# Performance work log

Hardware: AMD Instinct MI355X
Metric: run time of the kernel (lower is better)

The kernel has to match this reference:

```python
import jax, jax.numpy as jnp
import numpy as np

GWIDTH2 = 0.3  # Gaussian bandwidth squared
PNORM = 2


def setup_inputs() -> dict:
    key = jax.random.key(0)
    k1, k2 = jax.random.split(key)
    b, c, h, w = 16, 3, 256, 256
    npro = 32
    x = jax.random.uniform(k1, (b, c, h, w), dtype=jnp.float32)  # pixel values in [0,1]
    P = jax.random.uniform(k2, (npro, c), dtype=jnp.float32)     # p x c prototype pixels
    return {"x": x, "P": P}


def reference(x, P):
    # x: (b, c, h, w); P: (p, c)
    b, c, h, w = x.shape
    # broadcast difference -> (b, p, c, h, w); pnorm=2 distance over channels
    diff = x[:, None, :, :, :] - P[None, :, :, None, None]
    normsp = jnp.sum(diff ** PNORM, axis=2) ** (1.0 / PNORM)  # (b, p, h, w)
    expo = jnp.exp(-normsp / (2.0 * GWIDTH2))
    Y = jnp.sum(expo, axis=(2, 3))  # (b, p)
    return Y / (h * w)
```

## Files before the change

kernel.cpp:

```cpp
#include <hip/hip_runtime.h>


#define NPRO    32
#define HW      65536
#define THREADS 256
#define BPB     64
#define POISON  0xAAAAAAAAu

typedef float v2f __attribute__((ext_vector_type(2)));

__global__ __launch_bounds__(THREADS, 4) void soft_count_kernel(
    const float* __restrict__ x, const float* __restrict__ P,
    float* __restrict__ out)
{
    __shared__ float sPn[NPRO * 3];
    __shared__ float sred[4][NPRO];

    const float A = 2.4044917f;

    const int tid = threadIdx.x;
    if (tid < NPRO * 3) sPn[tid] = P[tid] * (-A);
    __syncthreads();

    const int b   = blockIdx.x / BPB;
    const int blk = blockIdx.x % BPB;

    const float* base = x + (size_t)b * 3 * HW;
    const int idx = blk * (THREADS * 4) + tid * 4;

    const float4 r4 = *(const float4*)(base + idx);
    const float4 g4 = *(const float4*)(base + HW + idx);
    const float4 b4 = *(const float4*)(base + 2 * HW + idx);

    const v2f Av = (v2f){A, A};
    v2f r2[2] = { (v2f){r4.x, r4.y}, (v2f){r4.z, r4.w} };
    v2f g2[2] = { (v2f){g4.x, g4.y}, (v2f){g4.z, g4.w} };
    v2f b2[2] = { (v2f){b4.x, b4.y}, (v2f){b4.z, b4.w} };

    v2f acc2[NPRO / 2];
#pragma unroll
    for (int p = 0; p < NPRO; ++p) {
        const float q0 = sPn[p * 3 + 0];
        const float q1 = sPn[p * 3 + 1];
        const float q2 = sPn[p * 3 + 2];
        const v2f P0 = (v2f){q0, q0};
        const v2f P1 = (v2f){q1, q1};
        const v2f P2 = (v2f){q2, q2};
        float s = 0.0f;
#pragma unroll
        for (int j = 0; j < 2; ++j) {
            const v2f d0 = __builtin_elementwise_fma(r2[j], Av, P0);
            const v2f d1 = __builtin_elementwise_fma(g2[j], Av, P1);
            const v2f d2 = __builtin_elementwise_fma(b2[j], Av, P2);
            v2f n2 = d0 * d0;
            n2 = __builtin_elementwise_fma(d1, d1, n2);
            n2 = __builtin_elementwise_fma(d2, d2, n2);
            s += __builtin_amdgcn_exp2f(-__builtin_amdgcn_sqrtf(n2.x));
            s += __builtin_amdgcn_exp2f(-__builtin_amdgcn_sqrtf(n2.y));
        }
        if (p & 1) acc2[p >> 1].y = s;
        else       acc2[p >> 1].x = s;
    }

    const int lane = tid & 63;
    const int wv   = tid >> 6;
#pragma unroll
    for (int q = 0; q < NPRO / 2; ++q) {
        v2f v = acc2[q];
#pragma unroll
        for (int off = 32; off >= 1; off >>= 1) {
            v2f o;
            o.x = __shfl_xor(v.x, off, 64);
            o.y = __shfl_xor(v.y, off, 64);
            v += o;
        }
        if (lane == 0) { sred[wv][2 * q] = v.x; sred[wv][2 * q + 1] = v.y; }
    }
    __syncthreads();

    if (tid < NPRO) {
        const float v = (sred[0][tid] + sred[1][tid] + sred[2][tid] + sred[3][tid])
                        * (1.0f / (float)HW);
        float* addr = &out[b * NPRO + tid];
        const unsigned int old =
            atomicCAS((unsigned int*)addr, POISON, __float_as_uint(v));
        if (old != POISON) atomicAdd(addr, v);
    }
}

extern "C" void kernel_launch(void* const* d_in, const int* in_sizes, int n_in,
                              void* d_out, int out_size, void* d_ws, size_t ws_size,
                              hipStream_t stream) {
    const float* x = (const float*)d_in[0];
    const float* P = (const float*)d_in[1];
    float* out = (float*)d_out;

    const int nb = in_sizes[0] / (3 * HW);

    soft_count_kernel<<<nb * BPB, THREADS, 0, stream>>>(x, P, out);
}
```

Measured before the change: 75.14 us.

## Expand squared distance algebraically and use transpose-style butterfly wave reduction

```diff
diff --git a/kernel.cpp b/kernel.cpp
--- a/kernel.cpp
+++ b/kernel.cpp
@@ -13,13 +13,23 @@
     const float* __restrict__ x, const float* __restrict__ P,
     float* __restrict__ out)
 {
-    __shared__ float sPn[NPRO * 3];
-    __shared__ float sred[4][NPRO];
+    __shared__ float4 sPC[NPRO];
+    __shared__ float  sred[4][NPRO];
 
     const float A = 2.4044917f;
 
     const int tid = threadIdx.x;
-    if (tid < NPRO * 3) sPn[tid] = P[tid] * (-A);
+    if (tid < NPRO) {
+        const float q0 = A * P[tid * 3 + 0];
+        const float q1 = A * P[tid * 3 + 1];
+        const float q2 = A * P[tid * 3 + 2];
+        float4 v;
+        v.x = -2.0f * q0;
+        v.y = -2.0f * q1;
+        v.z = -2.0f * q2;
+        v.w = q0 * q0 + q1 * q1 + q2 * q2;
+        sPC[tid] = v;
+    }
     __syncthreads();
 
     const int b   = blockIdx.x / BPB;
@@ -28,33 +38,42 @@
     const float* base = x + (size_t)b * 3 * HW;
     const int idx = blk * (THREADS * 4) + tid * 4;
 
-    const float4 r4 = *(const float4*)(base + idx);
-    const float4 g4 = *(const float4*)(base + HW + idx);
-    const float4 b4 = *(const float4*)(base + 2 * HW + idx);
+    const float4 rA = *(const float4*)(base + idx);
+    const float4 gA = *(const float4*)(base + HW + idx);
+    const float4 bA = *(const float4*)(base + 2 * HW + idx);
 
     const v2f Av = (v2f){A, A};
-    v2f r2[2] = { (v2f){r4.x, r4.y}, (v2f){r4.z, r4.w} };
-    v2f g2[2] = { (v2f){g4.x, g4.y}, (v2f){g4.z, g4.w} };
-    v2f b2[2] = { (v2f){b4.x, b4.y}, (v2f){b4.z, b4.w} };
+    v2f yr[2] = { (v2f){rA.x, rA.y} * Av, (v2f){rA.z, rA.w} * Av };
+    v2f yg[2] = { (v2f){gA.x, gA.y} * Av, (v2f){gA.z, gA.w} * Av };
+    v2f yb[2] = { (v2f){bA.x, bA.y} * Av, (v2f){bA.z, bA.w} * Av };
+
+    v2f m2[2];
+#pragma unroll
+    for (int j = 0; j < 2; ++j) {
+        v2f m = yr[j] * yr[j];
+        m = __builtin_elementwise_fma(yg[j], yg[j], m);
+        m = __builtin_elementwise_fma(yb[j], yb[j], m);
+        m2[j] = m;
+    }
+
+    const v2f Z2 = (v2f){0.0f, 0.0f};
 
     v2f acc2[NPRO / 2];
 #pragma unroll
     for (int p = 0; p < NPRO; ++p) {
-        const float q0 = sPn[p * 3 + 0];
-        const float q1 = sPn[p * 3 + 1];
-        const float q2 = sPn[p * 3 + 2];
-        const v2f P0 = (v2f){q0, q0};
-        const v2f P1 = (v2f){q1, q1};
-        const v2f P2 = (v2f){q2, q2};
+        const float4 pc = sPC[p];
+        const v2f U0 = (v2f){pc.x, pc.x};
+        const v2f U1 = (v2f){pc.y, pc.y};
+        const v2f U2 = (v2f){pc.z, pc.z};
+        const v2f Cc = (v2f){pc.w, pc.w};
         float s = 0.0f;
 #pragma unroll
         for (int j = 0; j < 2; ++j) {
-            const v2f d0 = __builtin_elementwise_fma(r2[j], Av, P0);
-            const v2f d1 = __builtin_elementwise_fma(g2[j], Av, P1);
-            const v2f d2 = __builtin_elementwise_fma(b2[j], Av, P2);
-            v2f n2 = d0 * d0;
-            n2 = __builtin_elementwise_fma(d1, d1, n2);
-            n2 = __builtin_elementwise_fma(d2, d2, n2);
+            v2f n2 = m2[j] + Cc;
+            n2 = __builtin_elementwise_fma(yr[j], U0, n2);
+            n2 = __builtin_elementwise_fma(yg[j], U1, n2);
+            n2 = __builtin_elementwise_fma(yb[j], U2, n2);
+            n2 = __builtin_elementwise_max(n2, Z2);
             s += __builtin_amdgcn_exp2f(-__builtin_amdgcn_sqrtf(n2.x));
             s += __builtin_amdgcn_exp2f(-__builtin_amdgcn_sqrtf(n2.y));
         }
@@ -64,18 +83,60 @@
 
     const int lane = tid & 63;
     const int wv   = tid >> 6;
+    const bool b0 = lane & 1, b1 = lane & 2, b2 = lane & 4, b3 = lane & 8,
+               b4 = lane & 16;
+
+    v2f t8[8];
 #pragma unroll
-    for (int q = 0; q < NPRO / 2; ++q) {
-        v2f v = acc2[q];
+    for (int i = 0; i < 8; ++i) {
+        const float sx = b0 ? acc2[i].x : acc2[i + 8].x;
+        const float sy = b0 ? acc2[i].y : acc2[i + 8].y;
+        const float kx = b0 ? acc2[i + 8].x : acc2[i].x;
+        const float ky = b0 ? acc2[i + 8].y : acc2[i].y;
+        t8[i].x = kx + __shfl_xor(sx, 1, 64);
+        t8[i].y = ky + __shfl_xor(sy, 1, 64);
+    }
+    v2f t4[4];
 #pragma unroll
-        for (int off = 32; off >= 1; off >>= 1) {
-            v2f o;
-            o.x = __shfl_xor(v.x, off, 64);
-            o.y = __shfl_xor(v.y, off, 64);
-            v += o;
-        }
-        if (lane == 0) { sred[wv][2 * q] = v.x; sred[wv][2 * q + 1] = v.y; }
+    for (int i = 0; i < 4; ++i) {
+        const float sx = b1 ? t8[i].x : t8[i + 4].x;
+        const float sy = b1 ? t8[i].y : t8[i + 4].y;
+        const float kx = b1 ? t8[i + 4].x : t8[i].x;
+        const float ky = b1 ? t8[i + 4].y : t8[i].y;
+        t4[i].x = kx + __shfl_xor(sx, 2, 64);
+        t4[i].y = ky + __shfl_xor(sy, 2, 64);
     }
+    v2f t2[2];
+#pragma unroll
+    for (int i = 0; i < 2; ++i) {
+        const float sx = b2 ? t4[i].x : t4[i + 2].x;
+        const float sy = b2 ? t4[i].y : t4[i + 2].y;
+        const float kx = b2 ? t4[i + 2].x : t4[i].x;
+        const float ky = b2 ? t4[i + 2].y : t4[i].y;
+        t2[i].x = kx + __shfl_xor(sx, 4, 64);
+        t2[i].y = ky + __shfl_xor(sy, 4, 64);
+    }
+    v2f t1;
+    {
+        const float sx = b3 ? t2[0].x : t2[1].x;
+        const float sy = b3 ? t2[0].y : t2[1].y;
+        const float kx = b3 ? t2[1].x : t2[0].x;
+        const float ky = b3 ? t2[1].y : t2[0].y;
+        t1.x = kx + __shfl_xor(sx, 8, 64);
+        t1.y = ky + __shfl_xor(sy, 8, 64);
+    }
+    float s;
+    {
+        const float snd = b4 ? t1.x : t1.y;
+        const float kp  = b4 ? t1.y : t1.x;
+        s = kp + __shfl_xor(snd, 16, 64);
+    }
+    s += __shfl_xor(s, 32, 64);
+
+    const int q = ((lane & 1) * 8) + (((lane >> 1) & 1) * 4)
+                + (((lane >> 2) & 1) * 2) + ((lane >> 3) & 1);
+    const int proto = 2 * q + ((lane >> 4) & 1);
+    if (lane < 32) sred[wv][proto] = s;
     __syncthreads();
 
     if (tid < NPRO) {
```

New measurement: 73.14 us. -2.7%, faster.
